# Performance work log

Hardware: AMD Instinct MI355X
Metric: run time of the kernel (lower is better)

Reference implementation:

```python
import jax, jax.numpy as jnp
import numpy as np
import math

HEADS = 16
D_MODEL = 1024
D_K = D_MODEL // HEADS


def setup_inputs() -> dict:
    key = jax.random.key(0)
    ks = jax.random.split(key, 11)
    B, S = 2, 2048
    s = 1.0 / math.sqrt(D_MODEL)
    return {
        "q": jax.random.normal(ks[0], (B, S, D_MODEL), jnp.float32),
        "k": jax.random.normal(ks[1], (B, S, D_MODEL), jnp.float32),
        "v": jax.random.normal(ks[2], (B, S, D_MODEL), jnp.float32),
        "Wq": jax.random.normal(ks[3], (D_MODEL, D_MODEL), jnp.float32) * s,
        "bq": jax.random.normal(ks[4], (D_MODEL,), jnp.float32) * s,
        "Wk": jax.random.normal(ks[5], (D_MODEL, D_MODEL), jnp.float32) * s,
        "bk": jax.random.normal(ks[6], (D_MODEL,), jnp.float32) * s,
        "Wv": jax.random.normal(ks[7], (D_MODEL, D_MODEL), jnp.float32) * s,
        "bv": jax.random.normal(ks[8], (D_MODEL,), jnp.float32) * s,
        "Wo": jax.random.normal(ks[9], (D_MODEL, D_MODEL), jnp.float32) * s,
        "bo": jax.random.normal(ks[10], (D_MODEL,), jnp.float32) * s,
    }


def reference(q, k, v, Wq, bq, Wk, bk, Wv, bv, Wo, bo):
    B, S, _ = q.shape
    # linear projections, split heads: [B, H, S, d_k]
    def proj(x, W, b):
        y = x @ W.T + b
        return y.reshape(B, -1, HEADS, D_K).transpose(0, 2, 1, 3)
    qh, kh, vh = proj(q, Wq, bq), proj(k, Wk, bk), proj(v, Wv, bv)
    # abs-modified scaled dot-product attention (no mask, eval -> no dropout)
    scores = jnp.abs(jnp.einsum("bhsd,bhtd->bhst", qh, kh) / math.sqrt(D_K))
    attn = jax.nn.softmax(scores, axis=-1)
    out = jnp.einsum("bhst,bhtd->bhsd", attn, vh)
    concat = out.transpose(0, 2, 1, 3).reshape(B, S, D_MODEL)
    return concat @ Wo.T + bo
```

## Files before the change

kernel.cpp:

```cpp
#include <hip/hip_runtime.h>
#include <hip/hip_bf16.h>

#define HEADS 16
#define DK 64
#define DM 1024
#define SEQ 2048
#define BATCH 2

using bf16x8 = __attribute__((ext_vector_type(8))) short;
using short4v = __attribute__((ext_vector_type(4))) short;
using f32x4 = __attribute__((ext_vector_type(4))) float;

static __device__ __forceinline__ short f2bf(float x) {
  union { float f; unsigned u; } c;
  c.f = x;
  unsigned r = (c.u + 0x7FFFu + ((c.u >> 16) & 1u)) >> 16;
  return (short)r;
}

static __device__ __forceinline__ unsigned pk2bf(float lo, float hi) {
  union { __hip_bfloat162 h; unsigned u; } c;
  c.h = __float22bfloat162_rn(float2{lo, hi});
  return c.u;
}

static __device__ __forceinline__ void gload_lds16(const void* g, void* l) {
  __builtin_amdgcn_global_load_lds(
      (const __attribute__((address_space(1))) void*)g,
      (__attribute__((address_space(3))) void*)l, 16, 0, 0);
}

__global__ __launch_bounds__(256) void cvt7(
    const float* __restrict__ s0, const float* __restrict__ s1,
    const float* __restrict__ s2, const float* __restrict__ s3,
    const float* __restrict__ s4, const float* __restrict__ s5,
    const float* __restrict__ s6, short* d0, short* d1, short* d2, short* d3,
    short* d4, short* d5, short* d6) {
  const int y = blockIdx.y;
  const float* s;
  short* d;
  int n;
  switch (y) {
    case 0: s = s0; d = d0; n = BATCH * SEQ * DM; break;
    case 1: s = s1; d = d1; n = BATCH * SEQ * DM; break;
    case 2: s = s2; d = d2; n = BATCH * SEQ * DM; break;
    case 3: s = s3; d = d3; n = DM * DM; break;
    case 4: s = s4; d = d4; n = DM * DM; break;
    case 5: s = s5; d = d5; n = DM * DM; break;
    default: s = s6; d = d6; n = DM * DM; break;
  }
  const int n4 = n >> 2;
  const int stride = gridDim.x * 256;
  for (int i = blockIdx.x * 256 + threadIdx.x; i < n4; i += stride) {
    float4 v = ((const float4*)s)[i];
    short4v o;
    o.x = f2bf(v.x);
    o.y = f2bf(v.y);
    o.z = f2bf(v.z);
    o.w = f2bf(v.w);
    ((short4v*)d)[i] = o;
  }
}

__global__ __launch_bounds__(256) void proj_qkv(
    const short* __restrict__ Aq, const short* __restrict__ Ak,
    const short* __restrict__ Av, const short* __restrict__ Wq_,
    const short* __restrict__ Wk_, const short* __restrict__ Wv_,
    const float* __restrict__ bq, const float* __restrict__ bk,
    const float* __restrict__ bv, short* __restrict__ Qh,
    short* __restrict__ Kh, short* __restrict__ Vt) {
  __shared__ short smem[128 * 136];
  short* As = smem;
  short* Ws = smem + 8192;

  const int z = blockIdx.z;
  const short* A = z == 0 ? Aq : z == 1 ? Ak : Av;
  const short* W = z == 0 ? Wq_ : z == 1 ? Wk_ : Wv_;
  const float* bias = z == 0 ? bq : z == 1 ? bk : bv;
  short* C = z == 0 ? Qh : z == 1 ? Kh : Vt;
  const bool tr = (z == 2);

  const int tid = threadIdx.x;
  const int wave = tid >> 6, lane = tid & 63;
  const int quad = lane >> 4, l15 = lane & 15;
  const int n0 = blockIdx.x * 128, m0 = blockIdx.y * 128;
  const int mh = (wave & 1) * 64, nh = (wave >> 1) * 64;
  const int ldr = lane >> 3, ldc = lane & 7;

  f32x4 acc[4][4] = {};

  for (int k0 = 0; k0 < 1024; k0 += 64) {
    __syncthreads();
#pragma unroll
    for (int i = 0; i < 8; ++i) {
      int seg = wave * 8 + i;
      int r = (seg & 15) * 8 + ldr;
      int kb = ldc ^ (r & 7);
      if (seg < 16)
        gload_lds16(&A[(size_t)(m0 + r) * 1024 + k0 + kb * 8], &As[seg * 512]);
      else
        gload_lds16(&W[(size_t)(n0 + r) * 1024 + k0 + kb * 8],
                    &Ws[(seg - 16) * 512]);
    }
    __syncthreads();
#pragma unroll
    for (int ks = 0; ks < 2; ++ks) {
      bf16x8 a[4], b[4];
      int kb = ks * 4 + quad;
#pragma unroll
      for (int f = 0; f < 4; ++f) {
        int rm = mh + f * 16 + l15;
        int rn = nh + f * 16 + l15;
        a[f] = *(const bf16x8*)&As[rm * 64 + (kb ^ (rm & 7)) * 8];
        b[f] = *(const bf16x8*)&Ws[rn * 64 + (kb ^ (rn & 7)) * 8];
      }
#pragma unroll
      for (int mf = 0; mf < 4; ++mf)
#pragma unroll
        for (int nf = 0; nf < 4; ++nf)
          acc[mf][nf] = __builtin_amdgcn_mfma_f32_16x16x32_bf16(
              a[mf], b[nf], acc[mf][nf], 0, 0, 0);
    }
  }

  float bvv[4];
#pragma unroll
  for (int nf = 0; nf < 4; ++nf) bvv[nf] = bias[n0 + nh + nf * 16 + l15];

  __syncthreads();
  short* Cb = smem;

  if (!tr) {
    const float osc = (z == 0) ? 0.18033688011112042f : 1.0f;
#pragma unroll
    for (int mf = 0; mf < 4; ++mf)
#pragma unroll
      for (int nf = 0; nf < 4; ++nf)
#pragma unroll
        for (int r = 0; r < 4; ++r)
          Cb[(mh + mf * 16 + quad * 4 + r) * 136 + nh + nf * 16 + l15] =
              f2bf((acc[mf][nf][r] + bvv[nf]) * osc);
    __syncthreads();
#pragma unroll
    for (int j = 0; j < 8; ++j) {
      int cid = tid + 256 * j;
      int row = cid >> 4, cb = cid & 15;
      bf16x8 v = *(const bf16x8*)&Cb[row * 136 + cb * 8];
      int m = m0 + row, n = n0 + cb * 8;
      int b = m >> 11, s = m & (SEQ - 1), h = n >> 6, d = n & 63;
      *(bf16x8*)&C[((size_t)(b * HEADS + h) * SEQ + s) * DK + d] = v;
    }
  } else {
#pragma unroll
    for (int mf = 0; mf < 4; ++mf)
#pragma unroll
      for (int nf = 0; nf < 4; ++nf) {
        short4v p;
        p.x = f2bf(acc[mf][nf][0] + bvv[nf]);
        p.y = f2bf(acc[mf][nf][1] + bvv[nf]);
        p.z = f2bf(acc[mf][nf][2] + bvv[nf]);
        p.w = f2bf(acc[mf][nf][3] + bvv[nf]);
        *(short4v*)&Cb[(nh + nf * 16 + l15) * 136 + mh + mf * 16 + quad * 4] =
            p;
      }
    __syncthreads();
#pragma unroll
    for (int j = 0; j < 8; ++j) {
      int cid = tid + 256 * j;
      int row = cid >> 4, cb = cid & 15;
      bf16x8 v = *(const bf16x8*)&Cb[row * 136 + cb * 8];
      int n = n0 + row, m = m0 + cb * 8;
      int b = m >> 11, s = m & (SEQ - 1), h = n >> 6, d = n & 63;
      *(bf16x8*)&C[((size_t)(b * HEADS + h) * DK + d) * SEQ + s] = v;
    }
  }
}

__global__ __launch_bounds__(256) void proj_out(const short* __restrict__ A,
                                                const short* __restrict__ W,
                                                const float* __restrict__ bias,
                                                float* __restrict__ C) {
  __shared__ short smem[128 * 136];
  short* As = smem;
  short* Ws = smem + 8192;

  const int tid = threadIdx.x;
  const int wave = tid >> 6, lane = tid & 63;
  const int quad = lane >> 4, l15 = lane & 15;
  const int n0 = blockIdx.x * 128, m0 = blockIdx.y * 128;
  const int mh = (wave & 1) * 64, nh = (wave >> 1) * 64;
  const int ldr = lane >> 3, ldc = lane & 7;

  f32x4 acc[4][4] = {};

  for (int k0 = 0; k0 < 1024; k0 += 64) {
    __syncthreads();
#pragma unroll
    for (int i = 0; i < 8; ++i) {
      int seg = wave * 8 + i;
      int r = (seg & 15) * 8 + ldr;
      int kb = ldc ^ (r & 7);
      if (seg < 16)
        gload_lds16(&A[(size_t)(m0 + r) * 1024 + k0 + kb * 8], &As[seg * 512]);
      else
        gload_lds16(&W[(size_t)(n0 + r) * 1024 + k0 + kb * 8],
                    &Ws[(seg - 16) * 512]);
    }
    __syncthreads();
#pragma unroll
    for (int ks = 0; ks < 2; ++ks) {
      bf16x8 a[4], b[4];
      int kb = ks * 4 + quad;
#pragma unroll
      for (int f = 0; f < 4; ++f) {
        int rm = mh + f * 16 + l15;
        int rn = nh + f * 16 + l15;
        a[f] = *(const bf16x8*)&As[rm * 64 + (kb ^ (rm & 7)) * 8];
        b[f] = *(const bf16x8*)&Ws[rn * 64 + (kb ^ (rn & 7)) * 8];
      }
#pragma unroll
      for (int mf = 0; mf < 4; ++mf)
#pragma unroll
        for (int nf = 0; nf < 4; ++nf)
          acc[mf][nf] = __builtin_amdgcn_mfma_f32_16x16x32_bf16(
              a[mf], b[nf], acc[mf][nf], 0, 0, 0);
    }
  }

  float bvv[4];
#pragma unroll
  for (int nf = 0; nf < 4; ++nf) bvv[nf] = bias[n0 + nh + nf * 16 + l15];
#pragma unroll
  for (int mf = 0; mf < 4; ++mf)
#pragma unroll
    for (int nf = 0; nf < 4; ++nf)
#pragma unroll
      for (int r = 0; r < 4; ++r)
        C[(size_t)(m0 + mh + mf * 16 + quad * 4 + r) * 1024 + n0 + nh +
          nf * 16 + l15] = acc[mf][nf][r] + bvv[nf];
}

__global__ __launch_bounds__(512, 4) void attn_mfma(
    const short* __restrict__ Qh, const short* __restrict__ Kh,
    const short* __restrict__ VtG, short* __restrict__ concat) {
  __shared__ __align__(16) short smem[4 * 64 * 64];
  __shared__ float Lsm[128];
  short* Kbuf = smem;
  short* Vbuf = smem + 2 * 4096;

  const int tid = threadIdx.x;
  const int wave = tid >> 6, lane = tid & 63;
  const int quad = lane >> 4, l15 = lane & 15;
  const int wq = wave & 3;
  const int wg = wave >> 2;
  const int bh = blockIdx.y;
  const int q0 = blockIdx.x * 128;
  const size_t base = (size_t)bh * SEQ * DK;
  const int ldr = lane >> 3, ldc = lane & 7;
  const int NT = SEQ / 64;

  bf16x8 qf[2][2];
#pragma unroll
  for (int mf = 0; mf < 2; ++mf)
#pragma unroll
    for (int ks = 0; ks < 2; ++ks)
      qf[mf][ks] =
          *(const bf16x8*)&Qh[base +
                              (size_t)(q0 + wq * 32 + mf * 16 + l15) * 64 +
                              ks * 32 + quad * 8];

  bf16x8 ones;
#pragma unroll
  for (int i = 0; i < 8; ++i) ones[i] = (short)0x3F80;

  f32x4 O[2][4] = {};
  f32x4 Lacc[2] = {};

  int krow[2];
#pragma unroll
  for (int kfl = 0; kfl < 2; ++kfl)
    krow[kfl] = 32 * wg + 8 * (l15 >> 2) + 4 * kfl + (l15 & 3);

  auto stage = [&](int kt, int buf) {
    int r = wave * 8 + ldr;
    int kswz = (r & 7) ^ (((r >> 3) & 3) << 1);
    gload_lds16(&Kh[base + (size_t)(kt * 64 + r) * 64 + (ldc ^ kswz) * 8],
                &Kbuf[buf * 4096 + wave * 512]);
    gload_lds16(&VtG[base + (size_t)r * SEQ + kt * 64 + (ldc ^ (r & 7)) * 8],
                &Vbuf[buf * 4096 + wave * 512]);
  };

  stage(0, 0);
  __syncthreads();

  int cur = 0;
  for (int kt = 0; kt < NT; ++kt) {
    if (kt + 1 < NT) stage(kt + 1, cur ^ 1);

    const short* Ks = &Kbuf[cur * 4096];
    const short* Vs = &Vbuf[cur * 4096];

    f32x4 sf[2][2] = {};
#pragma unroll
    for (int ks = 0; ks < 2; ++ks) {
      bf16x8 kfr[2];
      int kb = ks * 4 + quad;
#pragma unroll
      for (int kfl = 0; kfl < 2; ++kfl) {
        int n = krow[kfl];
        int kswz = (n & 7) ^ (((n >> 3) & 3) << 1);
        kfr[kfl] = *(const bf16x8*)&Ks[n * 64 + ((kb ^ kswz) << 3)];
      }
      __builtin_amdgcn_s_setprio(1);
#pragma unroll
      for (int kfl = 0; kfl < 2; ++kfl)
#pragma unroll
        for (int mf = 0; mf < 2; ++mf)
          sf[mf][kfl] = __builtin_amdgcn_mfma_f32_16x16x32_bf16(
              kfr[kfl], qf[mf][ks], sf[mf][kfl], 0, 0, 0);
      __builtin_amdgcn_s_setprio(0);
    }

    bf16x8 pa[2];
#pragma unroll
    for (int mf = 0; mf < 2; ++mf) {
      float e[8];
#pragma unroll
      for (int kfl = 0; kfl < 2; ++kfl)
#pragma unroll
        for (int r = 0; r < 4; ++r)
          e[kfl * 4 + r] = __builtin_amdgcn_exp2f(fabsf(sf[mf][kfl][r]));
      union { unsigned u[4]; bf16x8 v; } t;
      t.u[0] = pk2bf(e[0], e[1]);
      t.u[1] = pk2bf(e[2], e[3]);
      t.u[2] = pk2bf(e[4], e[5]);
      t.u[3] = pk2bf(e[6], e[7]);
      pa[mf] = t.v;
    }

    {
      int gb = wg * 4 + quad;
      bf16x8 bvf[4];
#pragma unroll
      for (int nf = 0; nf < 4; ++nf) {
        int d = nf * 16 + l15;
        bvf[nf] = *(const bf16x8*)&Vs[d * 64 + ((gb ^ (d & 7)) << 3)];
      }
      __builtin_amdgcn_s_setprio(1);
#pragma unroll
      for (int mf = 0; mf < 2; ++mf) {
#pragma unroll
        for (int nf = 0; nf < 4; ++nf)
          O[mf][nf] = __builtin_amdgcn_mfma_f32_16x16x32_bf16(
              pa[mf], bvf[nf], O[mf][nf], 0, 0, 0);
        Lacc[mf] = __builtin_amdgcn_mfma_f32_16x16x32_bf16(pa[mf], ones,
                                                           Lacc[mf], 0, 0, 0);
      }
      __builtin_amdgcn_s_setprio(0);
    }

    __syncthreads();
    cur ^= 1;
  }

  float* Osm = (float*)smem;
  if (wg == 1) {
#pragma unroll
    for (int mf = 0; mf < 2; ++mf)
#pragma unroll
      for (int nf = 0; nf < 4; ++nf) {
        int d = nf * 16 + l15;
        int rowb = (wq * 32 + mf * 16 + quad * 4) ^ ((d & 7) << 2);
        *(f32x4*)&Osm[d * 128 + rowb] = O[mf][nf];
      }
    if (l15 == 0)
#pragma unroll
      for (int mf = 0; mf < 2; ++mf)
#pragma unroll
        for (int r = 0; r < 4; ++r)
          Lsm[wq * 32 + mf * 16 + quad * 4 + r] = Lacc[mf][r];
  }
  __syncthreads();

  float inv_[2][4];
  if (wg == 0) {
#pragma unroll
    for (int mf = 0; mf < 2; ++mf)
#pragma unroll
      for (int nf = 0; nf < 4; ++nf) {
        int d = nf * 16 + l15;
        int rowb = (wq * 32 + mf * 16 + quad * 4) ^ ((d & 7) << 2);
        O[mf][nf] += *(const f32x4*)&Osm[d * 128 + rowb];
      }
#pragma unroll
    for (int mf = 0; mf < 2; ++mf)
#pragma unroll
      for (int r = 0; r < 4; ++r)
        inv_[mf][r] =
            1.f / (Lacc[mf][r] + Lsm[wq * 32 + mf * 16 + quad * 4 + r]);
  }
  __syncthreads();

  short* Es = smem;
  if (wg == 0) {
#pragma unroll
    for (int mf = 0; mf < 2; ++mf)
#pragma unroll
      for (int nf = 0; nf < 4; ++nf)
#pragma unroll
        for (int r = 0; r < 4; ++r) {
          int rw = wq * 32 + mf * 16 + quad * 4 + r;
          int d = nf * 16 + l15;
          Es[rw * 64 + (((d >> 3) ^ (rw & 7)) << 3) + (d & 7)] =
              f2bf(O[mf][nf][r] * inv_[mf][r]);
        }
  }
  __syncthreads();
  const int b = bh >> 4, h = bh & 15;
#pragma unroll
  for (int j = 0; j < 2; ++j) {
    int cid = tid + 512 * j;
    int rw = cid >> 3, g = cid & 7;
    bf16x8 v = *(const bf16x8*)&Es[rw * 64 + ((g ^ (rw & 7)) << 3)];
    *(bf16x8*)&concat[((size_t)(b * SEQ + q0 + rw)) * DM + h * 64 + g * 8] = v;
  }
}

extern "C" void kernel_launch(void* const* d_in, const int* in_sizes, int n_in,
                              void* d_out, int out_size, void* d_ws,
                              size_t ws_size, hipStream_t stream) {
  const float* q = (const float*)d_in[0];
  const float* k = (const float*)d_in[1];
  const float* v = (const float*)d_in[2];
  const float* Wq = (const float*)d_in[3];
  const float* bq = (const float*)d_in[4];
  const float* Wk = (const float*)d_in[5];
  const float* bk = (const float*)d_in[6];
  const float* Wv = (const float*)d_in[7];
  const float* bv = (const float*)d_in[8];
  const float* Wo = (const float*)d_in[9];
  const float* bo = (const float*)d_in[10];

  short* ws = (short*)d_ws;
  const size_t T4 = (size_t)BATCH * SEQ * DM;
  const size_t T1 = (size_t)DM * DM;
  short* qb = ws;
  short* kb_ = ws + T4;
  short* vb = ws + 2 * T4;
  short* Wqb = ws + 3 * T4;
  short* Wkb = Wqb + T1;
  short* Wvb = Wqb + 2 * T1;
  short* Wob = Wqb + 3 * T1;
  short* Qh = Wqb + 4 * T1;
  short* Kh = Qh + T4;
  short* VtG = Qh + 2 * T4;
  short* cc = Qh + 3 * T4;

  cvt7<<<dim3(1024, 7), 256, 0, stream>>>(q, k, v, Wq, Wk, Wv, Wo, qb, kb_, vb,
                                          Wqb, Wkb, Wvb, Wob);

  proj_qkv<<<dim3(DM / 128, (BATCH * SEQ) / 128, 3), 256, 0, stream>>>(
      qb, kb_, vb, Wqb, Wkb, Wvb, bq, bk, bv, Qh, Kh, VtG);

  attn_mfma<<<dim3(SEQ / 128, BATCH * HEADS), 512, 0, stream>>>(Qh, Kh, VtG,
                                                                cc);

  proj_out<<<dim3(DM / 128, (BATCH * SEQ) / 128), 256, 0, stream>>>(
      cc, Wob, bo, (float*)d_out);
}
```

Measured before the change: 225.2 us.

## Halve GEMM M tile to 64 and swizzle attention block mapping

Projection GEMMs use 64x128 output tiles instead of 128x128, doubling the number of blocks so the CUs are better filled, at the cost of lower arithmetic intensity per block. The transposed V epilogue uses a narrower staging stride to match. The attention kernel remaps its linear block index so that neighbouring blocks land on different heads, spreading K/V reuse across cache partitions.

```diff
diff --git a/kernel.cpp b/kernel.cpp
--- a/kernel.cpp
+++ b/kernel.cpp
@@ -69,9 +69,9 @@
     const float* __restrict__ bq, const float* __restrict__ bk,
     const float* __restrict__ bv, short* __restrict__ Qh,
     short* __restrict__ Kh, short* __restrict__ Vt) {
-  __shared__ short smem[128 * 136];
+  __shared__ short smem[12288];
   short* As = smem;
-  short* Ws = smem + 8192;
+  short* Ws = smem + 4096;
 
   const int z = blockIdx.z;
   const short* A = z == 0 ? Aq : z == 1 ? Ak : Av;
@@ -83,39 +83,45 @@
   const int tid = threadIdx.x;
   const int wave = tid >> 6, lane = tid & 63;
   const int quad = lane >> 4, l15 = lane & 15;
-  const int n0 = blockIdx.x * 128, m0 = blockIdx.y * 128;
-  const int mh = (wave & 1) * 64, nh = (wave >> 1) * 64;
+  const int n0 = blockIdx.x * 128, m0 = blockIdx.y * 64;
+  const int mh = (wave & 1) * 32, nh = (wave >> 1) * 64;
   const int ldr = lane >> 3, ldc = lane & 7;
 
-  f32x4 acc[4][4] = {};
+  f32x4 acc[2][4] = {};
 
   for (int k0 = 0; k0 < 1024; k0 += 64) {
     __syncthreads();
 #pragma unroll
-    for (int i = 0; i < 8; ++i) {
-      int seg = wave * 8 + i;
-      int r = (seg & 15) * 8 + ldr;
-      int kb = ldc ^ (r & 7);
-      if (seg < 16)
+    for (int i = 0; i < 6; ++i) {
+      int seg = wave * 6 + i;
+      if (seg < 8) {
+        int r = seg * 8 + ldr;
+        int kb = ldc ^ (r & 7);
         gload_lds16(&A[(size_t)(m0 + r) * 1024 + k0 + kb * 8], &As[seg * 512]);
-      else
+      } else {
+        int r = (seg - 8) * 8 + ldr;
+        int kb = ldc ^ (r & 7);
         gload_lds16(&W[(size_t)(n0 + r) * 1024 + k0 + kb * 8],
-                    &Ws[(seg - 16) * 512]);
+                    &Ws[(seg - 8) * 512]);
+      }
     }
     __syncthreads();
 #pragma unroll
     for (int ks = 0; ks < 2; ++ks) {
-      bf16x8 a[4], b[4];
+      bf16x8 a[2], b[4];
       int kb = ks * 4 + quad;
 #pragma unroll
+      for (int f = 0; f < 2; ++f) {
+        int rm = mh + f * 16 + l15;
+        a[f] = *(const bf16x8*)&As[rm * 64 + (kb ^ (rm & 7)) * 8];
+      }
+#pragma unroll
       for (int f = 0; f < 4; ++f) {
-        int rm = mh + f * 16 + l15;
         int rn = nh + f * 16 + l15;
-        a[f] = *(const bf16x8*)&As[rm * 64 + (kb ^ (rm & 7)) * 8];
         b[f] = *(const bf16x8*)&Ws[rn * 64 + (kb ^ (rn & 7)) * 8];
       }
 #pragma unroll
-      for (int mf = 0; mf < 4; ++mf)
+      for (int mf = 0; mf < 2; ++mf)
 #pragma unroll
         for (int nf = 0; nf < 4; ++nf)
           acc[mf][nf] = __builtin_amdgcn_mfma_f32_16x16x32_bf16(
@@ -133,7 +139,7 @@
   if (!tr) {
     const float osc = (z == 0) ? 0.18033688011112042f : 1.0f;
 #pragma unroll
-    for (int mf = 0; mf < 4; ++mf)
+    for (int mf = 0; mf < 2; ++mf)
 #pragma unroll
       for (int nf = 0; nf < 4; ++nf)
 #pragma unroll
@@ -142,7 +148,7 @@
               f2bf((acc[mf][nf][r] + bvv[nf]) * osc);
     __syncthreads();
 #pragma unroll
-    for (int j = 0; j < 8; ++j) {
+    for (int j = 0; j < 4; ++j) {
       int cid = tid + 256 * j;
       int row = cid >> 4, cb = cid & 15;
       bf16x8 v = *(const bf16x8*)&Cb[row * 136 + cb * 8];
@@ -152,7 +158,7 @@
     }
   } else {
 #pragma unroll
-    for (int mf = 0; mf < 4; ++mf)
+    for (int mf = 0; mf < 2; ++mf)
 #pragma unroll
       for (int nf = 0; nf < 4; ++nf) {
         short4v p;
@@ -160,15 +166,15 @@
         p.y = f2bf(acc[mf][nf][1] + bvv[nf]);
         p.z = f2bf(acc[mf][nf][2] + bvv[nf]);
         p.w = f2bf(acc[mf][nf][3] + bvv[nf]);
-        *(short4v*)&Cb[(nh + nf * 16 + l15) * 136 + mh + mf * 16 + quad * 4] =
+        *(short4v*)&Cb[(nh + nf * 16 + l15) * 72 + mh + mf * 16 + quad * 4] =
             p;
       }
     __syncthreads();
 #pragma unroll
-    for (int j = 0; j < 8; ++j) {
+    for (int j = 0; j < 4; ++j) {
       int cid = tid + 256 * j;
-      int row = cid >> 4, cb = cid & 15;
-      bf16x8 v = *(const bf16x8*)&Cb[row * 136 + cb * 8];
+      int row = cid >> 3, cb = cid & 7;
+      bf16x8 v = *(const bf16x8*)&Cb[row * 72 + cb * 8];
       int n = n0 + row, m = m0 + cb * 8;
       int b = m >> 11, s = m & (SEQ - 1), h = n >> 6, d = n & 63;
       *(bf16x8*)&C[((size_t)(b * HEADS + h) * DK + d) * SEQ + s] = v;
@@ -180,46 +186,52 @@
                                                 const short* __restrict__ W,
                                                 const float* __restrict__ bias,
                                                 float* __restrict__ C) {
-  __shared__ short smem[128 * 136];
+  __shared__ short smem[12288];
   short* As = smem;
-  short* Ws = smem + 8192;
+  short* Ws = smem + 4096;
 
   const int tid = threadIdx.x;
   const int wave = tid >> 6, lane = tid & 63;
   const int quad = lane >> 4, l15 = lane & 15;
-  const int n0 = blockIdx.x * 128, m0 = blockIdx.y * 128;
-  const int mh = (wave & 1) * 64, nh = (wave >> 1) * 64;
+  const int n0 = blockIdx.x * 128, m0 = blockIdx.y * 64;
+  const int mh = (wave & 1) * 32, nh = (wave >> 1) * 64;
   const int ldr = lane >> 3, ldc = lane & 7;
 
-  f32x4 acc[4][4] = {};
+  f32x4 acc[2][4] = {};
 
   for (int k0 = 0; k0 < 1024; k0 += 64) {
     __syncthreads();
 #pragma unroll
-    for (int i = 0; i < 8; ++i) {
-      int seg = wave * 8 + i;
-      int r = (seg & 15) * 8 + ldr;
-      int kb = ldc ^ (r & 7);
-      if (seg < 16)
+    for (int i = 0; i < 6; ++i) {
+      int seg = wave * 6 + i;
+      if (seg < 8) {
+        int r = seg * 8 + ldr;
+        int kb = ldc ^ (r & 7);
         gload_lds16(&A[(size_t)(m0 + r) * 1024 + k0 + kb * 8], &As[seg * 512]);
-      else
+      } else {
+        int r = (seg - 8) * 8 + ldr;
+        int kb = ldc ^ (r & 7);
         gload_lds16(&W[(size_t)(n0 + r) * 1024 + k0 + kb * 8],
-                    &Ws[(seg - 16) * 512]);
+                    &Ws[(seg - 8) * 512]);
+      }
     }
     __syncthreads();
 #pragma unroll
     for (int ks = 0; ks < 2; ++ks) {
-      bf16x8 a[4], b[4];
+      bf16x8 a[2], b[4];
       int kb = ks * 4 + quad;
 #pragma unroll
+      for (int f = 0; f < 2; ++f) {
+        int rm = mh + f * 16 + l15;
+        a[f] = *(const bf16x8*)&As[rm * 64 + (kb ^ (rm & 7)) * 8];
+      }
+#pragma unroll
       for (int f = 0; f < 4; ++f) {
-        int rm = mh + f * 16 + l15;
         int rn = nh + f * 16 + l15;
-        a[f] = *(const bf16x8*)&As[rm * 64 + (kb ^ (rm & 7)) * 8];
         b[f] = *(const bf16x8*)&Ws[rn * 64 + (kb ^ (rn & 7)) * 8];
       }
 #pragma unroll
-      for (int mf = 0; mf < 4; ++mf)
+      for (int mf = 0; mf < 2; ++mf)
 #pragma unroll
         for (int nf = 0; nf < 4; ++nf)
           acc[mf][nf] = __builtin_amdgcn_mfma_f32_16x16x32_bf16(
@@ -231,7 +243,7 @@
 #pragma unroll
   for (int nf = 0; nf < 4; ++nf) bvv[nf] = bias[n0 + nh + nf * 16 + l15];
 #pragma unroll
-  for (int mf = 0; mf < 4; ++mf)
+  for (int mf = 0; mf < 2; ++mf)
 #pragma unroll
     for (int nf = 0; nf < 4; ++nf)
 #pragma unroll
@@ -253,8 +265,10 @@
   const int quad = lane >> 4, l15 = lane & 15;
   const int wq = wave & 3;
   const int wg = wave >> 2;
-  const int bh = blockIdx.y;
-  const int q0 = blockIdx.x * 128;
+  const int lin = blockIdx.x + (blockIdx.y << 4);
+  const int o = ((lin & 7) << 6) + (lin >> 3);
+  const int bh = o >> 4;
+  const int q0 = (o & 15) * 128;
   const size_t base = (size_t)bh * SEQ * DK;
   const int ldr = lane >> 3, ldc = lane & 7;
   const int NT = SEQ / 64;
@@ -459,12 +473,12 @@
   cvt7<<<dim3(1024, 7), 256, 0, stream>>>(q, k, v, Wq, Wk, Wv, Wo, qb, kb_, vb,
                                           Wqb, Wkb, Wvb, Wob);
 
-  proj_qkv<<<dim3(DM / 128, (BATCH * SEQ) / 128, 3), 256, 0, stream>>>(
+  proj_qkv<<<dim3(DM / 128, (BATCH * SEQ) / 64, 3), 256, 0, stream>>>(
       qb, kb_, vb, Wqb, Wkb, Wvb, bq, bk, bv, Qh, Kh, VtG);
 
   attn_mfma<<<dim3(SEQ / 128, BATCH * HEADS), 512, 0, stream>>>(Qh, Kh, VtG,
                                                                 cc);
 
-  proj_out<<<dim3(DM / 128, (BATCH * SEQ) / 128), 256, 0, stream>>>(
+  proj_out<<<dim3(DM / 128, (BATCH * SEQ) / 64), 256, 0, stream>>>(
       cc, Wob, bo, (float*)d_out);
 }
```

Measured after the change: 225.6 us. No clear change (+0.2%).
